# Performance work log

Measured on AMD Instinct MI355X. Metric: run time of the kernel, lower is better.

## Reference

```python
import jax, jax.numpy as jnp
import numpy as np

DIM = 64
POS_HID = 64
ATTN_HID = DIM * 4  # attn_mlp_hidden_mult = 4
B, N = 4, 512


def setup_inputs() -> dict:
    key = jax.random.key(0)
    ks = jax.random.split(key, 12)
    s = lambda fan_in: 1.0 / np.sqrt(fan_in)
    return {
        "x": jax.random.normal(ks[0], (B, N, DIM), dtype=jnp.float32),
        "pos": jax.random.normal(ks[1], (B, N, 3), dtype=jnp.float32),
        # to_qkv: Linear(dim, 3*dim, bias=False); stored as [in, out]
        "w_qkv": jax.random.uniform(ks[2], (DIM, 3 * DIM), jnp.float32, -s(DIM), s(DIM)),
        # pos_mlp: Linear(3, POS_HID) -> ReLU -> Linear(POS_HID, dim)
        "pos_w1": jax.random.uniform(ks[3], (3, POS_HID), jnp.float32, -s(3), s(3)),
        "pos_b1": jax.random.uniform(ks[4], (POS_HID,), jnp.float32, -s(3), s(3)),
        "pos_w2": jax.random.uniform(ks[5], (POS_HID, DIM), jnp.float32, -s(POS_HID), s(POS_HID)),
        "pos_b2": jax.random.uniform(ks[6], (DIM,), jnp.float32, -s(POS_HID), s(POS_HID)),
        # attn_mlp: Linear(dim, ATTN_HID) -> ReLU -> Linear(ATTN_HID, 1)
        "attn_w1": jax.random.uniform(ks[7], (DIM, ATTN_HID), jnp.float32, -s(DIM), s(DIM)),
        "attn_b1": jax.random.uniform(ks[8], (ATTN_HID,), jnp.float32, -s(DIM), s(DIM)),
        "attn_w2": jax.random.uniform(ks[9], (ATTN_HID, 1), jnp.float32, -s(ATTN_HID), s(ATTN_HID)),
        "attn_b2": jax.random.uniform(ks[10], (1,), jnp.float32, -s(ATTN_HID), s(ATTN_HID)),
    }


def reference(x, pos, w_qkv, pos_w1, pos_b1, pos_w2, pos_b2,
              attn_w1, attn_b1, attn_w2, attn_b2):
    # qkv projection: [b,n,3d] -> q,k,v each [b,n,d]
    qkv = x @ w_qkv
    q, k, v = jnp.split(qkv, 3, axis=-1)
    # pairwise relative positions: [b,n,n,3]
    rel_pos = pos[:, :, None, :] - pos[:, None, :, :]
    # pos_mlp: [b,n,n,d]
    rel_pos_emb = jax.nn.relu(rel_pos @ pos_w1 + pos_b1) @ pos_w2 + pos_b2
    # pairwise q-k differences: [b,n,n,d]
    qk_rel = q[:, :, None, :] - k[:, None, :, :]
    # attn_mlp -> scalar sim per pair: [b,n,n]
    h = qk_rel + rel_pos_emb
    sim = (jax.nn.relu(h @ attn_w1 + attn_b1) @ attn_w2 + attn_b2)[..., 0]
    attn = jax.nn.softmax(sim, axis=-1)
    # values augmented by positional embedding, weighted sum over j
    v_aug = v[:, None, :, :] + rel_pos_emb  # [b,n,n,d]
    agg = jnp.einsum('bij,bijd->bid', attn, v_aug)
    return agg
```

## Files before the change

kernel.cpp:

```cpp
#include <hip/hip_runtime.h>
#include <hip/hip_bf16.h>
#include <stdint.h>

#define DIM 64
#define TH  256
#define NN  512
#define IB  4

typedef __attribute__((ext_vector_type(8))) short bf16x8;
typedef __attribute__((ext_vector_type(4))) float f32x4;

__device__ __forceinline__ short f2bf(float f) {
    union { float f; uint32_t u; } v; v.f = f;
    uint32_t r = v.u + 0x7fffu + ((v.u >> 16) & 1u);
    return (short)(r >> 16);
}

__global__ void prep_all(const float* __restrict__ x, const float* __restrict__ w_qkv,
                         const float* __restrict__ attn_w1,
                         const float* __restrict__ pos_w2, const float* __restrict__ pos_b2,
                         const float* __restrict__ attn_b1,
                         float* __restrict__ V, float* __restrict__ QW1, short* __restrict__ Kneg,
                         short* __restrict__ Bg, float* __restrict__ cbg) {
    const int tid = threadIdx.x;
    if (blockIdx.x >= 256) {
        const int t = (blockIdx.x - 256) * 32 + (tid >> 3);
        const int h0 = (tid & 7) * 8;
        #pragma unroll
        for (int hh = 0; hh < 8; hh++) {
            int h = h0 + hh;
            float m = 0.f;
            for (int d = 0; d < DIM; d++) m += pos_w2[h * DIM + d] * attn_w1[d * TH + t];
            Bg[t * 128 + h] = f2bf(m);
            Bg[t * 128 + 64 + h] = f2bf(attn_w1[h * TH + t]);
        }
        if ((tid & 7) == 0) {
            float cb = attn_b1[t];
            for (int d = 0; d < DIM; d++) cb += pos_b2[d] * attn_w1[d * TH + t];
            cbg[t] = cb;
        }
        return;
    }
    const int b = blockIdx.x >> 6, j0 = (blockIdx.x & 63) * 8;
    __shared__ float xs[8][DIM], qs[8][DIM];
    #pragma unroll
    for (int p = 0; p < 2; p++) {
        int idx = tid + p * 256;
        xs[idx >> 6][idx & 63] = x[(size_t)(b * NN + j0) * DIM + idx];
    }
    __syncthreads();
    if (tid < 192) {
        for (int jj = 0; jj < 8; jj++) {
            float acc = 0.f;
            for (int e = 0; e < DIM; e++) acc += xs[jj][e] * w_qkv[e * 192 + tid];
            size_t row = (size_t)(b * NN + j0 + jj) * DIM;
            if (tid < 64)       qs[jj][tid] = acc;
            else if (tid < 128) Kneg[row + (tid - 64)] = f2bf(-acc);
            else                V[row + (tid - 128)] = acc;
        }
    }
    __syncthreads();
    for (int jj = 0; jj < 8; jj++) {
        float aq = 0.f;
        for (int d = 0; d < DIM; d++) aq += qs[jj][d] * attn_w1[d * TH + tid];
        QW1[(size_t)(b * NN + j0 + jj) * TH + tid] = aq;
    }
}

__launch_bounds__(512, 2)
__global__ void ptl_main(const float* __restrict__ pos, const float* __restrict__ pos_w1,
                         const float* __restrict__ pos_b1, const float* __restrict__ pos_w2,
                         const float* __restrict__ pos_b2, const float* __restrict__ attn_w2,
                         const float* __restrict__ V, const float* __restrict__ QW1,
                         const short* __restrict__ Kneg, const short* __restrict__ Bg,
                         const float* __restrict__ cbg, float* __restrict__ out) {
    const int b = blockIdx.x >> 7, i0 = (blockIdx.x & 127) * IB;
    const int tid = threadIdx.x;
    const int wv = tid >> 6, lane = tid & 63;
    const int lhi = lane >> 4, llo = lane & 15;

    __shared__ __align__(16) short Blds[TH * 128];
    __shared__ float posl[NN][3];
    __shared__ float2 qwl[IB][TH];
    __shared__ float4 pw4[DIM];
    __shared__ float simbuf[IB][NN];
    __shared__ float aggw[8][IB][2][DIM];
    __shared__ float fin[IB][2][DIM];
    __shared__ float wred[2][IB][8];

    for (int idx = tid; idx < TH * 16; idx += 512) {
        int t = idx >> 4, s = idx & 15;
        *(uint4*)((char*)Blds + t * 256 + ((s ^ (t & 15)) << 4)) =
            *(const uint4*)((const char*)Bg + (size_t)idx * 16);
    }
    for (int idx = tid; idx < NN * 3; idx += 512)
        ((float*)posl)[idx] = pos[b * NN * 3 + idx];
    if (tid < TH) {
        float w2 = attn_w2[tid], cb = cbg[tid];
        #pragma unroll
        for (int ii = 0; ii < IB; ii++) {
            float2 q2; q2.x = QW1[(size_t)(b * NN + i0 + ii) * TH + tid] + cb; q2.y = w2;
            qwl[ii][tid] = q2;
        }
    }
    if (tid < DIM) {
        float4 w; w.x = pos_w1[tid]; w.y = pos_w1[DIM + tid];
        w.z = pos_w1[2 * DIM + tid]; w.w = pos_b1[tid];
        pw4[tid] = w;
    }
    bf16x8 knf[4][2];
    #pragma unroll
    for (int jt = 0; jt < 4; jt++) {
        size_t row = (size_t)(b * NN + wv * 64 + jt * 16 + llo) * DIM;
        knf[jt][0] = *(const bf16x8*)(Kneg + row + lhi * 8);
        knf[jt][1] = *(const bf16x8*)(Kneg + row + 32 + lhi * 8);
    }
    __syncthreads();

    const char* mb = (const char*)Blds + llo * 256;
    const int s0 = ((0  + lhi) ^ llo) << 4;
    const int s1 = ((4  + lhi) ^ llo) << 4;
    const int s2 = ((8  + lhi) ^ llo) << 4;
    const int s3 = ((12 + lhi) ^ llo) << 4;

    #pragma unroll 1
    for (int ii = 0; ii < IB; ii++) {
        const float pi0 = posl[i0 + ii][0], pi1 = posl[i0 + ii][1], pi2 = posl[i0 + ii][2];
        bf16x8 gfr[4][2];
        #pragma unroll
        for (int jt = 0; jt < 4; jt++) {
            const int jA = wv * 64 + jt * 16 + llo;
            const float r0 = pi0 - posl[jA][0], r1 = pi1 - posl[jA][1], r2 = pi2 - posl[jA][2];
            #pragma unroll
            for (int kk = 0; kk < 2; kk++) {
                #pragma unroll
                for (int e2 = 0; e2 < 4; e2++) {
                    float4 wA = pw4[kk * 32 + lhi * 8 + 2 * e2];
                    float4 wB = pw4[kk * 32 + lhi * 8 + 2 * e2 + 1];
                    float2 p2;
                    p2.x = fmaxf(r0 * wA.x + r1 * wA.y + r2 * wA.z + wA.w, 0.f);
                    p2.y = fmaxf(r0 * wB.x + r1 * wB.y + r2 * wB.z + wB.w, 0.f);
                    union { __hip_bfloat162 h2; uint32_t u; } cv;
                    cv.h2 = __float22bfloat162_rn(p2);
                    ((uint32_t*)&gfr[jt][kk])[e2] = cv.u;
                }
            }
        }
        float sa[4][4] = {};
        #pragma unroll 4
        for (int tt = 0; tt < 16; tt++) {
            const int t = tt * 16 + llo;
            bf16x8 bf0 = *(const bf16x8*)(mb + tt * 4096 + s0);
            bf16x8 bf1 = *(const bf16x8*)(mb + tt * 4096 + s1);
            bf16x8 bf2 = *(const bf16x8*)(mb + tt * 4096 + s2);
            bf16x8 bf3 = *(const bf16x8*)(mb + tt * 4096 + s3);
            const float2 qw = qwl[ii][t];
            #pragma unroll
            for (int jt = 0; jt < 4; jt++) {
                f32x4 acc = {0.f, 0.f, 0.f, 0.f};
                acc = __builtin_amdgcn_mfma_f32_16x16x32_bf16(gfr[jt][0], bf0, acc, 0, 0, 0);
                acc = __builtin_amdgcn_mfma_f32_16x16x32_bf16(gfr[jt][1], bf1, acc, 0, 0, 0);
                acc = __builtin_amdgcn_mfma_f32_16x16x32_bf16(knf[jt][0], bf2, acc, 0, 0, 0);
                acc = __builtin_amdgcn_mfma_f32_16x16x32_bf16(knf[jt][1], bf3, acc, 0, 0, 0);
                #pragma unroll
                for (int r = 0; r < 4; r++)
                    sa[jt][r] += fmaxf(acc[r] + qw.x, 0.f) * qw.y;
            }
        }
        #pragma unroll
        for (int jt = 0; jt < 4; jt++) {
            #pragma unroll
            for (int r = 0; r < 4; r++) {
                float v = sa[jt][r];
                v += __shfl_xor(v, 1); v += __shfl_xor(v, 2);
                v += __shfl_xor(v, 4); v += __shfl_xor(v, 8);
                if (llo == 0) simbuf[ii][wv * 64 + jt * 16 + lhi * 4 + r] = v;
            }
        }
    }
    __syncthreads();

    float sv[IB];
    #pragma unroll
    for (int ii = 0; ii < IB; ii++) {
        float s = simbuf[ii][tid];
        sv[ii] = s;
        float mx = s;
        #pragma unroll
        for (int off = 1; off < 64; off <<= 1) mx = fmaxf(mx, __shfl_xor(mx, off));
        if (lane == 0) wred[0][ii][wv] = mx;
    }
    __syncthreads();
    float pv[IB];
    #pragma unroll
    for (int ii = 0; ii < IB; ii++) {
        float bm = wred[0][ii][0];
        #pragma unroll
        for (int w = 1; w < 8; w++) bm = fmaxf(bm, wred[0][ii][w]);
        float p = __expf(sv[ii] - bm);
        pv[ii] = p;
        float ps = p;
        #pragma unroll
        for (int off = 1; off < 64; off <<= 1) ps += __shfl_xor(ps, off);
        if (lane == 0) wred[1][ii][wv] = ps;
    }
    __syncthreads();
    #pragma unroll
    for (int ii = 0; ii < IB; ii++) {
        float den = 0.f;
        #pragma unroll
        for (int w = 0; w < 8; w++) den += wred[1][ii][w];
        simbuf[ii][tid] = pv[ii] / den;
    }
    __syncthreads();

    {
        const int d = lane;
        const float4 wd = pw4[d];
        float pia[IB][3];
        #pragma unroll
        for (int ii = 0; ii < IB; ii++) {
            pia[ii][0] = posl[i0 + ii][0]; pia[ii][1] = posl[i0 + ii][1]; pia[ii][2] = posl[i0 + ii][2];
        }
        float av[IB] = {}, ag[IB] = {};
        const float* vb = V + (size_t)(b * NN + wv * 64) * DIM + d;
        #pragma unroll 4
        for (int jj = 0; jj < 64; jj++) {
            const int j = wv * 64 + jj;
            const float vv = vb[jj * DIM];
            const float p0 = posl[j][0], p1 = posl[j][1], p2 = posl[j][2];
            #pragma unroll
            for (int ii = 0; ii < IB; ii++) {
                const float a = simbuf[ii][j];
                av[ii] += a * vv;
                float g = (pia[ii][0] - p0) * wd.x + (pia[ii][1] - p1) * wd.y +
                          (pia[ii][2] - p2) * wd.z + wd.w;
                ag[ii] += a * fmaxf(g, 0.f);
            }
        }
        #pragma unroll
        for (int ii = 0; ii < IB; ii++) {
            aggw[wv][ii][0][d] = av[ii];
            aggw[wv][ii][1][d] = ag[ii];
        }
    }
    __syncthreads();
    {
        const int ii = tid >> 7, pp = (tid >> 6) & 1, d2 = tid & 63;
        float s = 0.f;
        #pragma unroll
        for (int w = 0; w < 8; w++) s += aggw[w][ii][pp][d2];
        fin[ii][pp][d2] = s;
    }
    __syncthreads();
    if (tid < IB * DIM) {
        const int ii = tid >> 6, d2 = tid & 63;
        float o = fin[ii][0][d2] + pos_b2[d2];
        for (int h = 0; h < DIM; h++) o += fin[ii][1][h] * pos_w2[h * DIM + d2];
        out[(size_t)(b * NN + i0 + ii) * DIM + d2] = o;
    }
}

extern "C" void kernel_launch(void* const* d_in, const int* in_sizes, int n_in,
                              void* d_out, int out_size, void* d_ws, size_t ws_size,
                              hipStream_t stream) {
    const float* x       = (const float*)d_in[0];
    const float* pos     = (const float*)d_in[1];
    const float* w_qkv   = (const float*)d_in[2];
    const float* pos_w1  = (const float*)d_in[3];
    const float* pos_b1  = (const float*)d_in[4];
    const float* pos_w2  = (const float*)d_in[5];
    const float* pos_b2  = (const float*)d_in[6];
    const float* attn_w1 = (const float*)d_in[7];
    const float* attn_b1 = (const float*)d_in[8];
    const float* attn_w2 = (const float*)d_in[9];

    char* ws = (char*)d_ws;
    short* Bg   = (short*)(ws + 0);
    float* cbg  = (float*)(ws + 65536);
    float* Vw   = (float*)(ws + 66560);
    float* QW1  = (float*)(ws + 590848);
    short* Kneg = (short*)(ws + 2688000);

    float* outp = (float*)d_out;

    prep_all<<<264, 256, 0, stream>>>(x, w_qkv, attn_w1, pos_w2, pos_b2, attn_b1,
                                      Vw, QW1, Kneg, Bg, cbg);
    ptl_main<<<4 * (NN / IB), 512, 0, stream>>>(pos, pos_w1, pos_b1, pos_w2, pos_b2,
                                                attn_w2, Vw, QW1, Kneg, Bg, cbg, outp);
}
```

Baseline: 210.6 us.

## Split hidden-dim weight staging into halves to cut LDS and raise occupancy

The main kernel now stages only half of the 256-row fused weight matrix in shared memory at a time, processing hidden units in two passes and accumulating partial similarity scores into simbuf. This halves the weight LDS footprint so the launch bound can request 4 blocks per CU instead of 2. In exchange the per-block position-MLP fragments are recomputed twice and an extra barrier plus reload is added. The prep kernel's loops are also reordered to accumulate 8 outputs per thread, reusing each global weight load.

```diff
diff --git a/kernel.cpp b/kernel.cpp
--- a/kernel.cpp
+++ b/kernel.cpp
@@ -26,13 +26,16 @@
     if (blockIdx.x >= 256) {
         const int t = (blockIdx.x - 256) * 32 + (tid >> 3);
         const int h0 = (tid & 7) * 8;
+        float m[8] = {};
+        for (int d = 0; d < DIM; d++) {
+            float wa1 = attn_w1[d * TH + t];
+            #pragma unroll
+            for (int hh = 0; hh < 8; hh++) m[hh] += pos_w2[(h0 + hh) * DIM + d] * wa1;
+        }
         #pragma unroll
         for (int hh = 0; hh < 8; hh++) {
-            int h = h0 + hh;
-            float m = 0.f;
-            for (int d = 0; d < DIM; d++) m += pos_w2[h * DIM + d] * attn_w1[d * TH + t];
-            Bg[t * 128 + h] = f2bf(m);
-            Bg[t * 128 + 64 + h] = f2bf(attn_w1[h * TH + t]);
+            Bg[t * 128 + h0 + hh] = f2bf(m[hh]);
+            Bg[t * 128 + 64 + h0 + hh] = f2bf(attn_w1[(h0 + hh) * TH + t]);
         }
         if ((tid & 7) == 0) {
             float cb = attn_b1[t];
@@ -50,24 +53,33 @@
     }
     __syncthreads();
     if (tid < 192) {
+        float acc[8] = {};
+        for (int e = 0; e < DIM; e++) {
+            float wq = w_qkv[e * 192 + tid];
+            #pragma unroll
+            for (int jj = 0; jj < 8; jj++) acc[jj] += xs[jj][e] * wq;
+        }
+        #pragma unroll
         for (int jj = 0; jj < 8; jj++) {
-            float acc = 0.f;
-            for (int e = 0; e < DIM; e++) acc += xs[jj][e] * w_qkv[e * 192 + tid];
             size_t row = (size_t)(b * NN + j0 + jj) * DIM;
-            if (tid < 64)       qs[jj][tid] = acc;
-            else if (tid < 128) Kneg[row + (tid - 64)] = f2bf(-acc);
-            else                V[row + (tid - 128)] = acc;
-        }
-    }
-    __syncthreads();
-    for (int jj = 0; jj < 8; jj++) {
-        float aq = 0.f;
-        for (int d = 0; d < DIM; d++) aq += qs[jj][d] * attn_w1[d * TH + tid];
-        QW1[(size_t)(b * NN + j0 + jj) * TH + tid] = aq;
-    }
+            if (tid < 64)       qs[jj][tid] = acc[jj];
+            else if (tid < 128) Kneg[row + (tid - 64)] = f2bf(-acc[jj]);
+            else                V[row + (tid - 128)] = acc[jj];
+        }
+    }
+    __syncthreads();
+    float aq[8] = {};
+    for (int d = 0; d < DIM; d++) {
+        float w = attn_w1[d * TH + tid];
+        #pragma unroll
+        for (int jj = 0; jj < 8; jj++) aq[jj] += qs[jj][d] * w;
+    }
+    #pragma unroll
+    for (int jj = 0; jj < 8; jj++)
+        QW1[(size_t)(b * NN + j0 + jj) * TH + tid] = aq[jj];
 }
 
-__launch_bounds__(512, 2)
+__launch_bounds__(512, 4)
 __global__ void ptl_main(const float* __restrict__ pos, const float* __restrict__ pos_w1,
                          const float* __restrict__ pos_b1, const float* __restrict__ pos_w2,
                          const float* __restrict__ pos_b2, const float* __restrict__ attn_w2,
@@ -79,7 +91,7 @@
     const int wv = tid >> 6, lane = tid & 63;
     const int lhi = lane >> 4, llo = lane & 15;
 
-    __shared__ __align__(16) short Blds[TH * 128];
+    __shared__ __align__(16) short Blds[128 * 128];
     __shared__ float posl[NN][3];
     __shared__ float2 qwl[IB][TH];
     __shared__ float4 pw4[DIM];
@@ -88,11 +100,6 @@
     __shared__ float fin[IB][2][DIM];
     __shared__ float wred[2][IB][8];
 
-    for (int idx = tid; idx < TH * 16; idx += 512) {
-        int t = idx >> 4, s = idx & 15;
-        *(uint4*)((char*)Blds + t * 256 + ((s ^ (t & 15)) << 4)) =
-            *(const uint4*)((const char*)Bg + (size_t)idx * 16);
-    }
     for (int idx = tid; idx < NN * 3; idx += 512)
         ((float*)posl)[idx] = pos[b * NN * 3 + idx];
     if (tid < TH) {
@@ -124,57 +131,72 @@
     const int s3 = ((12 + lhi) ^ llo) << 4;
 
     #pragma unroll 1
-    for (int ii = 0; ii < IB; ii++) {
-        const float pi0 = posl[i0 + ii][0], pi1 = posl[i0 + ii][1], pi2 = posl[i0 + ii][2];
-        bf16x8 gfr[4][2];
-        #pragma unroll
-        for (int jt = 0; jt < 4; jt++) {
-            const int jA = wv * 64 + jt * 16 + llo;
-            const float r0 = pi0 - posl[jA][0], r1 = pi1 - posl[jA][1], r2 = pi2 - posl[jA][2];
-            #pragma unroll
-            for (int kk = 0; kk < 2; kk++) {
+    for (int half = 0; half < 2; half++) {
+        if (half) __syncthreads();
+        for (int idx = tid; idx < 128 * 16; idx += 512) {
+            int t = idx >> 4, s = idx & 15;
+            *(uint4*)((char*)Blds + t * 256 + ((s ^ (t & 15)) << 4)) =
+                *(const uint4*)((const char*)Bg + ((size_t)half * 2048 + idx) * 16);
+        }
+        __syncthreads();
+
+        #pragma unroll 1
+        for (int ii = 0; ii < IB; ii++) {
+            const float pi0 = posl[i0 + ii][0], pi1 = posl[i0 + ii][1], pi2 = posl[i0 + ii][2];
+            bf16x8 gfr[4][2];
+            #pragma unroll
+            for (int jt = 0; jt < 4; jt++) {
+                const int jA = wv * 64 + jt * 16 + llo;
+                const float r0 = pi0 - posl[jA][0], r1 = pi1 - posl[jA][1], r2 = pi2 - posl[jA][2];
                 #pragma unroll
-                for (int e2 = 0; e2 < 4; e2++) {
-                    float4 wA = pw4[kk * 32 + lhi * 8 + 2 * e2];
-                    float4 wB = pw4[kk * 32 + lhi * 8 + 2 * e2 + 1];
-                    float2 p2;
-                    p2.x = fmaxf(r0 * wA.x + r1 * wA.y + r2 * wA.z + wA.w, 0.f);
-                    p2.y = fmaxf(r0 * wB.x + r1 * wB.y + r2 * wB.z + wB.w, 0.f);
-                    union { __hip_bfloat162 h2; uint32_t u; } cv;
-                    cv.h2 = __float22bfloat162_rn(p2);
-                    ((uint32_t*)&gfr[jt][kk])[e2] = cv.u;
+                for (int kk = 0; kk < 2; kk++) {
+                    #pragma unroll
+                    for (int e2 = 0; e2 < 4; e2++) {
+                        float4 wA = pw4[kk * 32 + lhi * 8 + 2 * e2];
+                        float4 wB = pw4[kk * 32 + lhi * 8 + 2 * e2 + 1];
+                        float2 p2;
+                        p2.x = fmaxf(r0 * wA.x + r1 * wA.y + r2 * wA.z + wA.w, 0.f);
+                        p2.y = fmaxf(r0 * wB.x + r1 * wB.y + r2 * wB.z + wB.w, 0.f);
+                        union { __hip_bfloat162 h2; uint32_t u; } cv;
+                        cv.h2 = __float22bfloat162_rn(p2);
+                        ((uint32_t*)&gfr[jt][kk])[e2] = cv.u;
+                    }
                 }
             }
-        }
-        float sa[4][4] = {};
-        #pragma unroll 4
-        for (int tt = 0; tt < 16; tt++) {
-            const int t = tt * 16 + llo;
-            bf16x8 bf0 = *(const bf16x8*)(mb + tt * 4096 + s0);
-            bf16x8 bf1 = *(const bf16x8*)(mb + tt * 4096 + s1);
-            bf16x8 bf2 = *(const bf16x8*)(mb + tt * 4096 + s2);
-            bf16x8 bf3 = *(const bf16x8*)(mb + tt * 4096 + s3);
-            const float2 qw = qwl[ii][t];
+            float sa[4][4] = {};
+            #pragma unroll 4
+            for (int tt = 0; tt < 8; tt++) {
+                const int t = half * 128 + tt * 16 + llo;
+                bf16x8 bf0 = *(const bf16x8*)(mb + tt * 4096 + s0);
+                bf16x8 bf1 = *(const bf16x8*)(mb + tt * 4096 + s1);
+                bf16x8 bf2 = *(const bf16x8*)(mb + tt * 4096 + s2);
+                bf16x8 bf3 = *(const bf16x8*)(mb + tt * 4096 + s3);
+                const float2 qw = qwl[ii][t];
+                #pragma unroll
+                for (int jt = 0; jt < 4; jt++) {
+                    f32x4 acc = {0.f, 0.f, 0.f, 0.f};
+                    acc = __builtin_amdgcn_mfma_f32_16x16x32_bf16(gfr[jt][0], bf0, acc, 0, 0, 0);
+                    acc = __builtin_amdgcn_mfma_f32_16x16x32_bf16(gfr[jt][1], bf1, acc, 0, 0, 0);
+                    acc = __builtin_amdgcn_mfma_f32_16x16x32_bf16(knf[jt][0], bf2, acc, 0, 0, 0);
+                    acc = __builtin_amdgcn_mfma_f32_16x16x32_bf16(knf[jt][1], bf3, acc, 0, 0, 0);
+                    #pragma unroll
+                    for (int r = 0; r < 4; r++)
+                        sa[jt][r] += fmaxf(acc[r] + qw.x, 0.f) * qw.y;
+                }
+            }
             #pragma unroll
             for (int jt = 0; jt < 4; jt++) {
-                f32x4 acc = {0.f, 0.f, 0.f, 0.f};
-                acc = __builtin_amdgcn_mfma_f32_16x16x32_bf16(gfr[jt][0], bf0, acc, 0, 0, 0);
-                acc = __builtin_amdgcn_mfma_f32_16x16x32_bf16(gfr[jt][1], bf1, acc, 0, 0, 0);
-                acc = __builtin_amdgcn_mfma_f32_16x16x32_bf16(knf[jt][0], bf2, acc, 0, 0, 0);
-                acc = __builtin_amdgcn_mfma_f32_16x16x32_bf16(knf[jt][1], bf3, acc, 0, 0, 0);
                 #pragma unroll
-                for (int r = 0; r < 4; r++)
-                    sa[jt][r] += fmaxf(acc[r] + qw.x, 0.f) * qw.y;
-            }
-        }
-        #pragma unroll
-        for (int jt = 0; jt < 4; jt++) {
-            #pragma unroll
-            for (int r = 0; r < 4; r++) {
-                float v = sa[jt][r];
-                v += __shfl_xor(v, 1); v += __shfl_xor(v, 2);
-                v += __shfl_xor(v, 4); v += __shfl_xor(v, 8);
-                if (llo == 0) simbuf[ii][wv * 64 + jt * 16 + lhi * 4 + r] = v;
+                for (int r = 0; r < 4; r++) {
+                    float v = sa[jt][r];
+                    v += __shfl_xor(v, 1); v += __shfl_xor(v, 2);
+                    v += __shfl_xor(v, 4); v += __shfl_xor(v, 8);
+                    if (llo == 0) {
+                        const int j = wv * 64 + jt * 16 + lhi * 4 + r;
+                        if (half == 0) simbuf[ii][j] = v;
+                        else           simbuf[ii][j] += v;
+                    }
+                }
             }
         }
     }
```

New measurement: 356.0 us. +69.0%, slower.
